# Kernel optimization log

Hardware: AMD Instinct MI355X
Metric: run time of the kernel (lower is better)

The kernel has to match this reference:

```python
import jax, jax.numpy as jnp
import numpy as np

L, d, D, X, B = 64, 2, 32, 2, 2048  # sites, local dim, bond dim, kraus dim, batch
STD = 0.01  # kernel_init = normal(stddev=0.01)


def setup_inputs() -> dict:
    key = jax.random.key(0)
    k1, k2, k3, k4 = jax.random.split(key, 4)
    # local quantum-number indices for (row, col) halves: shape [B, 2L]
    qn = jax.random.randint(k1, (B, 2 * L), 0, d, dtype=jnp.int32)
    # boundary tensors: random + all-ones boundary (as in setup())
    left = STD * jax.random.normal(k2, (d, D, X), jnp.float32) + jnp.ones((d, D, X), jnp.float32)
    right = STD * jax.random.normal(k3, (d, D, X), jnp.float32) + jnp.ones((d, D, X), jnp.float32)
    # middle tensors: random + identity on the (D,D) bond indices for every (site, s, kraus)
    iden = jnp.broadcast_to(jnp.eye(D, dtype=jnp.float32)[None, None, :, :, None], (L - 2, d, D, D, X))
    middle = STD * jax.random.normal(k4, (L - 2, d, D, D, X), jnp.float32) + iden
    return {"qn": qn, "left_tensors": left, "right_tensors": right, "middle_tensors": middle}


def _contract_mpdo(qn, left_tensors, right_tensors, middle_tensors):
    # qn: [2L] ints; split into row / column quantum numbers of the density matrix
    qn_r, qn_c = jnp.split(qn, 2, axis=-1)
    # left/right boundary edges: (D,X) @ (X,D) -> (D,D)
    left_edge = left_tensors[qn_r[0]] @ jnp.conj(left_tensors[qn_c[0]]).T
    right_edge = right_tensors[qn_r[-1]] @ jnp.conj(right_tensors[qn_c[-1]]).T

    @jax.checkpoint
    def step(edge, pair):
        tensor, sr, sc = pair  # tensor: (d,D,D,X)
        # (D,D,X) x (D,D) -> (D,X,D)
        tri = jnp.einsum('ijk,il->jkl', tensor[sr], edge)
        # (D,X,D) x (D,D,X) -> (D,D)
        new_edge = jnp.einsum('jkl,lmk->jm', tri, jnp.conj(tensor[sc]))
        return new_edge, None

    edge, _ = jax.lax.scan(step, left_edge, (middle_tensors, qn_r[1:-1], qn_c[1:-1]), unroll=1)
    return jnp.einsum('ij,ij->', edge, right_edge)


def reference(qn, left_tensors, right_tensors, middle_tensors):
    rho = jax.vmap(lambda q: _contract_mpdo(q, left_tensors, right_tensors, middle_tensors))(qn)
    return jnp.log(rho.astype(jnp.complex64))
```

## Files before the change

### kernel.cpp

```cpp
#include <hip/hip_runtime.h>
#include <hip/hip_bf16.h>
#include <math.h>


typedef __attribute__((ext_vector_type(8)))  short short8;
typedef __attribute__((ext_vector_type(16))) float f32x16;

#define EPITCH 33

static __device__ inline unsigned pk2(float lo, float hi) {
    union { __hip_bfloat162 h; unsigned u; } cv;
    cv.h = __float22bfloat162_rn(make_float2(lo, hi));
    return cv.u;
}
static __device__ inline short8 mk8(unsigned u0, unsigned u1, unsigned u2, unsigned u3) {
    union { short8 v; unsigned u[4]; } r;
    r.u[0] = u0; r.u[1] = u1; r.u[2] = u2; r.u[3] = u3;
    return r.v;
}
static __device__ inline short8 S8(uint4 u) {
    union { uint4 a; short8 v; } c; c.a = u; return c.v;
}
static __device__ inline void pl32swap(unsigned& x, unsigned& y) {
    asm("v_permlane32_swap_b32 %0, %1" : "+v"(x), "+v"(y));
}
static __device__ inline f32x16 MFMA(short8 a, short8 b, f32x16 c) {
    return __builtin_amdgcn_mfma_f32_32x32x16_bf16(a, b, c, 0, 0, 0);
}
static __device__ inline f32x16 zero16() {
    f32x16 z = {0.f,0.f,0.f,0.f,0.f,0.f,0.f,0.f,0.f,0.f,0.f,0.f,0.f,0.f,0.f,0.f};
    return z;
}

__global__ __launch_bounds__(256) void mpdo_prestage(
    const float* __restrict__ middle, unsigned* __restrict__ ws)
{
    const int site = blockIdx.x;
    const int t    = threadIdx.x;
    const int s    = t >> 7;
    const int h    = (t >> 6) & 1;
    const int hi   = (t >> 5) & 1;
    const int col  = t & 31;
    const float2* m2 = (const float2*)middle + (size_t)(site*2 + s) * 1024;
    float2 v[8];
    #pragma unroll
    for (int e = 0; e < 8; ++e) {
        const int kk = 16*h + 8*hi + e;
        float2 d = m2[kk*32 + col];
        if (kk == col) { d.x -= 1.f; d.y -= 1.f; }
        v[e] = d;
    }
    uint4 o0, o1;
    o0.x = pk2(v[0].x, v[1].x); o0.y = pk2(v[2].x, v[3].x);
    o0.z = pk2(v[4].x, v[5].x); o0.w = pk2(v[6].x, v[7].x);
    o1.x = pk2(v[0].y, v[1].y); o1.y = pk2(v[2].y, v[3].y);
    o1.z = pk2(v[4].y, v[5].y); o1.w = pk2(v[6].y, v[7].y);
    uint4* w4 = (uint4*)ws;
    const int lane_off = hi*32 + col;
    w4[((site*2 + s)*4 + 0 + h)*64 + lane_off] = o0;
    w4[((site*2 + s)*4 + 2 + h)*64 + lane_off] = o1;
}

#define SITE_BODY(CA, CB, NA, NB, SITE)                                          \
  {                                                                              \
        \
    float ef[16];                                                                \
    _Pragma("unroll")                                                            \
    for (int h = 0; h < 2; ++h) {                                                \
      const int base = col*EPITCH + 16*h + 8*hi;                                 \
      _Pragma("unroll")                                                          \
      for (int c = 0; c < 8; ++c) ef[h*8 + c] = Ew[base + c];                    \
    }                                                                            \
                                                  \
    short8 EB[2];                                                                \
    _Pragma("unroll")                                                            \
    for (int h = 0; h < 2; ++h) {                                                \
      unsigned ua = pk2(e[8*h+0], e[8*h+1]);                                     \
      unsigned ub = pk2(e[8*h+2], e[8*h+3]);                                     \
      unsigned uc = pk2(e[8*h+4], e[8*h+5]);                                     \
      unsigned ud = pk2(e[8*h+6], e[8*h+7]);                                     \
      pl32swap(ua, uc); pl32swap(ub, ud);                                        \
      EB[h] = mk8(ua, ub, uc, ud);                                               \
    }                                                                            \
                                                              \
    f32x16 acc0 = MFMA(S8(CA[0]), EB[0], zero16());                              \
    acc0 = MFMA(S8(CA[1]), EB[1], acc0);                                         \
    f32x16 acc1 = MFMA(S8(CA[2]), EB[0], zero16());                              \
    acc1 = MFMA(S8(CA[3]), EB[1], acc1);                                         \
                                                                    \
    short8 EA[2];                                                                \
    _Pragma("unroll")                                                            \
    for (int h = 0; h < 2; ++h)                                                  \
      EA[h] = mk8(pk2(ef[8*h+0], ef[8*h+1]), pk2(ef[8*h+2], ef[8*h+3]),          \
                  pk2(ef[8*h+4], ef[8*h+5]), pk2(ef[8*h+6], ef[8*h+7]));         \
                                                                \
    f32x16 V0 = MFMA(EA[0], S8(CB[0]), zero16());                                \
    V0 = MFMA(EA[1], S8(CB[1]), V0);                                             \
    f32x16 V1 = MFMA(EA[0], S8(CB[2]), zero16());                                \
    V1 = MFMA(EA[1], S8(CB[3]), V1);                                             \
                            \
    {                                                                            \
      const int pfi = ((SITE) < 62) ? (SITE) : 61;                               \
      const int ba = (pfi*2 + srn)*4, bb = (pfi*2 + scn)*4;                      \
      _Pragma("unroll")                                                          \
      for (int kh = 0; kh < 4; ++kh) {                                           \
        NA[kh] = w4g[(ba + kh)*64 + lane_off];                                   \
        NB[kh] = w4g[(bb + kh)*64 + lane_off];                                   \
      }                                                                          \
      const int qi = ((SITE) + 2 <= 62) ? (SITE) + 2 : 62;                       \
      srn = q[qi]; scn = q[qi + 64];                                             \
    }                                                                            \
                                             \
    _Pragma("unroll")                                                            \
    for (int h = 0; h < 2; ++h) {                                                \
      unsigned ua = pk2(V0[8*h+0], V0[8*h+1]);                                   \
      unsigned ub = pk2(V0[8*h+2], V0[8*h+3]);                                   \
      unsigned uc = pk2(V0[8*h+4], V0[8*h+5]);                                   \
      unsigned ud = pk2(V0[8*h+6], V0[8*h+7]);                                   \
      pl32swap(ua, uc); pl32swap(ub, ud);                                        \
      acc0 = MFMA(S8(CA[h]), mk8(ua, ub, uc, ud), acc0);                         \
    }                                                                            \
    _Pragma("unroll")                                                            \
    for (int h = 0; h < 2; ++h) {                                                \
      unsigned ua = pk2(V1[8*h+0], V1[8*h+1]);                                   \
      unsigned ub = pk2(V1[8*h+2], V1[8*h+3]);                                   \
      unsigned uc = pk2(V1[8*h+4], V1[8*h+5]);                                   \
      unsigned ud = pk2(V1[8*h+6], V1[8*h+7]);                                   \
      pl32swap(ua, uc); pl32swap(ub, ud);                                        \
      acc1 = MFMA(S8(CA[2+h]), mk8(ua, ub, uc, ud), acc1);                       \
    }                                                                            \
          \
    _Pragma("unroll")                                                            \
    for (int r = 0; r < 16; ++r)                                                 \
      e[r] = fmaf(2.f, e[r], (acc0[r] + acc1[r]) + (V0[r] + V1[r]));             \
    _Pragma("unroll")                                                            \
    for (int r = 0; r < 16; ++r) Ew[rowr[r]*EPITCH + col] = e[r];                \
  }

__global__ __launch_bounds__(256, 2) void mpdo_ws(
    const int*      __restrict__ qn,
    const float*    __restrict__ left,
    const float*    __restrict__ right,
    const unsigned* __restrict__ ws,
    float*          __restrict__ out,
    const int       cplx)
{
    __shared__ float E_all[4][32*EPITCH];

    const int t    = threadIdx.x;
    const int w    = t >> 6;
    const int lane = t & 63;
    const int hi   = lane >> 5;
    const int col  = lane & 31;
    const int elem = blockIdx.x * 4 + w;
    const int* q   = qn + (size_t)elem * 128;
    float* Ew = E_all[w];
    const int lane_off = hi*32 + col;
    const uint4* w4g = (const uint4*)ws;

    int rowr[16];
    #pragma unroll
    for (int r = 0; r < 16; ++r) rowr[r] = (r & 3) + 8*(r >> 2) + 4*hi;

    float e[16];
    {
        const float* Lr = left + (size_t)q[0]  * 64;
        const float* Lc = left + (size_t)q[64] * 64;
        const float c0v = Lc[col*2 + 0], c1v = Lc[col*2 + 1];
        #pragma unroll
        for (int r = 0; r < 16; ++r)
            e[r] = Lr[rowr[r]*2 + 0] * c0v + Lr[rowr[r]*2 + 1] * c1v;
    }
    #pragma unroll
    for (int r = 0; r < 16; ++r) Ew[rowr[r]*EPITCH + col] = e[r];

    uint4 CA[4], CB[4], NA[4], NB[4];
    {
        const int sr = q[1], sc = q[65];
        const int ba = sr*4, bb = sc*4;
        #pragma unroll
        for (int kh = 0; kh < 4; ++kh) {
            CA[kh] = w4g[(ba + kh)*64 + lane_off];
            CB[kh] = w4g[(bb + kh)*64 + lane_off];
        }
    }
    int srn = q[2], scn = q[66];

    #pragma unroll 1
    for (int it = 0; it < 31; ++it) {
        const int siteA = 2*it + 1;
        SITE_BODY(CA, CB, NA, NB, siteA)
        SITE_BODY(NA, NB, CA, CB, siteA + 1)
    }

    {
        const float* Rr = right + (size_t)q[63]  * 64;
        const float* Rc = right + (size_t)q[127] * 64;
        const float rc0 = Rc[col*2 + 0], rc1 = Rc[col*2 + 1];
        float part = 0.f;
        #pragma unroll
        for (int r = 0; r < 16; ++r) {
            const float re = Rr[rowr[r]*2 + 0]*rc0 + Rr[rowr[r]*2 + 1]*rc1;
            part += e[r] * re;
        }
        #pragma unroll
        for (int off = 32; off > 0; off >>= 1)
            part += __shfl_down(part, off, 64);
        if (lane == 0) {
            const float re = logf(fabsf(part));
            if (cplx) {
                out[2*elem + 0] = re;
                out[2*elem + 1] = (part < 0.f) ? 3.14159265358979323846f : 0.f;
            } else {
                out[elem] = re;
            }
        }
    }
}

__global__ __launch_bounds__(256, 2) void mpdo_mfma_fb(
    const int* __restrict__ qn, const float* __restrict__ left,
    const float* __restrict__ right, const float* __restrict__ middle,
    float* __restrict__ out, const int cplx)
{
    __shared__ unsigned mid_b[2048];
    __shared__ float    E_s[4][32*EPITCH];

    const int t = threadIdx.x, w = t >> 6, lane = t & 63;
    const int hi = lane >> 5, col = lane & 31;
    const int elem = blockIdx.x * 4 + w;
    const int* q = qn + (size_t)elem * 128;
    float* Ew = E_s[w];
    const int sp = (t >> 4) & 15, sj = t & 15, jj = sj * 2;
    const float dj = (sp == sj) ? 1.0f : 0.0f;
    const int v0 = (0 + 2*sp) * 16 + sj, v1 = (32 + 2*sp) * 16 + sj;

    int rowr[16];
    #pragma unroll
    for (int r = 0; r < 16; ++r) rowr[r] = (r & 3) + 8*(r >> 2) + 4*hi;

    float e[16];
    {
        const float* Lr = left + (size_t)q[0]  * 64;
        const float* Lc = left + (size_t)q[64] * 64;
        const float c0v = Lc[col*2 + 0], c1v = Lc[col*2 + 1];
        #pragma unroll
        for (int r = 0; r < 16; ++r)
            e[r] = Lr[rowr[r]*2 + 0] * c0v + Lr[rowr[r]*2 + 1] * c1v;
    }
    const float4* gm = (const float4*)middle;
    float4 A0 = gm[v0], A1 = gm[v0 + 16], B0 = gm[v1], B1 = gm[v1 + 16];
    int srn = q[1], scn = q[65];

    for (int site = 1; site <= 62; ++site) {
        {
            uint2* m2 = (uint2*)mid_b;
            m2[((0*16 + sp)*32 + jj) >> 1] = make_uint2(pk2(A0.x - dj, A1.x), pk2(A0.z, A1.z - dj));
            m2[((1*16 + sp)*32 + jj) >> 1] = make_uint2(pk2(A0.y - dj, A1.y), pk2(A0.w, A1.w - dj));
            m2[((2*16 + sp)*32 + jj) >> 1] = make_uint2(pk2(B0.x - dj, B1.x), pk2(B0.z, B1.z - dj));
            m2[((3*16 + sp)*32 + jj) >> 1] = make_uint2(pk2(B0.y - dj, B1.y), pk2(B0.w, B1.w - dj));
        }
        #pragma unroll
        for (int r = 0; r < 16; ++r) Ew[rowr[r]*EPITCH + col] = e[r];
        __syncthreads();
        const int sr = srn, sc = scn;
        if (site < 62) {
            const float4* gn = (const float4*)(middle + (size_t)site * 4096);
            A0 = gn[v0]; A1 = gn[v0 + 16]; B0 = gn[v1]; B1 = gn[v1 + 16];
            srn = q[site + 1]; scn = q[site + 65];
        }
        short8 aT[2][2], bF[2][2];
        #pragma unroll
        for (int k = 0; k < 2; ++k)
            #pragma unroll
            for (int h = 0; h < 2; ++h) {
                const int pa = ((sr*2 + k)*16 + 8*h + 4*hi) * 32 + col;
                aT[k][h] = mk8(mid_b[pa], mid_b[pa+32], mid_b[pa+64], mid_b[pa+96]);
                const int pb = ((sc*2 + k)*16 + 8*h + 4*hi) * 32 + col;
                bF[k][h] = mk8(mid_b[pb], mid_b[pb+32], mid_b[pb+64], mid_b[pb+96]);
            }
        short8 EA[2];
        #pragma unroll
        for (int h = 0; h < 2; ++h) {
            const int base = col*EPITCH + 16*h + 8*hi;
            EA[h] = mk8(pk2(Ew[base+0], Ew[base+1]), pk2(Ew[base+2], Ew[base+3]),
                        pk2(Ew[base+4], Ew[base+5]), pk2(Ew[base+6], Ew[base+7]));
        }
        short8 EB[2];
        #pragma unroll
        for (int h = 0; h < 2; ++h) {
            unsigned ua = pk2(e[8*h+0], e[8*h+1]);
            unsigned ub = pk2(e[8*h+2], e[8*h+3]);
            unsigned uc = pk2(e[8*h+4], e[8*h+5]);
            unsigned ud = pk2(e[8*h+6], e[8*h+7]);
            pl32swap(ua, uc); pl32swap(ub, ud);
            EB[h] = mk8(ua, ub, uc, ud);
        }
        f32x16 V0 = MFMA(EA[0], bF[0][0], zero16()); V0 = MFMA(EA[1], bF[0][1], V0);
        f32x16 V1 = MFMA(EA[0], bF[1][0], zero16()); V1 = MFMA(EA[1], bF[1][1], V1);
        f32x16 acc = MFMA(aT[0][0], EB[0], zero16());
        acc = MFMA(aT[0][1], EB[1], acc);
        acc = MFMA(aT[1][0], EB[0], acc);
        acc = MFMA(aT[1][1], EB[1], acc);
        #pragma unroll
        for (int k = 0; k < 2; ++k) {
            const f32x16& V = k ? V1 : V0;
            #pragma unroll
            for (int h = 0; h < 2; ++h) {
                unsigned ua = pk2(V[8*h+0], V[8*h+1]);
                unsigned ub = pk2(V[8*h+2], V[8*h+3]);
                unsigned uc = pk2(V[8*h+4], V[8*h+5]);
                unsigned ud = pk2(V[8*h+6], V[8*h+7]);
                pl32swap(ua, uc); pl32swap(ub, ud);
                acc = MFMA(aT[k][h], mk8(ua, ub, uc, ud), acc);
            }
        }
        #pragma unroll
        for (int r = 0; r < 16; ++r)
            e[r] = 2.0f*e[r] + acc[r] + V0[r] + V1[r];
        __syncthreads();
    }
    {
        const float* Rr = right + (size_t)q[63]  * 64;
        const float* Rc = right + (size_t)q[127] * 64;
        const float rc0 = Rc[col*2 + 0], rc1 = Rc[col*2 + 1];
        float part = 0.f;
        #pragma unroll
        for (int r = 0; r < 16; ++r)
            part += e[r] * (Rr[rowr[r]*2 + 0]*rc0 + Rr[rowr[r]*2 + 1]*rc1);
        #pragma unroll
        for (int off = 32; off > 0; off >>= 1)
            part += __shfl_down(part, off, 64);
        if (lane == 0) {
            const float re = logf(fabsf(part));
            if (cplx) { out[2*elem] = re; out[2*elem+1] = (part < 0.f) ? 3.14159265f : 0.f; }
            else      { out[elem] = re; }
        }
    }
}

extern "C" void kernel_launch(void* const* d_in, const int* in_sizes, int n_in,
                              void* d_out, int out_size, void* d_ws, size_t ws_size,
                              hipStream_t stream) {
    const int*   qn     = (const int*)  d_in[0];
    const float* left   = (const float*)d_in[1];
    const float* right  = (const float*)d_in[2];
    const float* middle = (const float*)d_in[3];
    float* out = (float*)d_out;

    const int B    = in_sizes[0] / 128;
    const int cplx = (out_size >= 2 * B) ? 1 : 0;
    const size_t need = 62ull * 8192ull;

    if (ws_size >= need) {
        mpdo_prestage<<<62, 256, 0, stream>>>(middle, (unsigned*)d_ws);
        mpdo_ws<<<B / 4, 256, 0, stream>>>(qn, left, right, (const unsigned*)d_ws,
                                           out, cplx);
    } else {
        mpdo_mfma_fb<<<B / 4, 256, 0, stream>>>(qn, left, right, middle, out, cplx);
    }
}
```

Baseline: 129.2 us.

## Carry edge and its transpose in registers instead of round-tripping through LDS

```diff
diff --git a/kernel.cpp b/kernel.cpp
--- a/kernel.cpp
+++ b/kernel.cpp
@@ -5,8 +5,6 @@
 
 typedef __attribute__((ext_vector_type(8)))  short short8;
 typedef __attribute__((ext_vector_type(16))) float f32x16;
-
-#define EPITCH 33
 
 static __device__ inline unsigned pk2(float lo, float hi) {
     union { __hip_bfloat162 h; unsigned u; } cv;
@@ -30,6 +28,28 @@
 static __device__ inline f32x16 zero16() {
     f32x16 z = {0.f,0.f,0.f,0.f,0.f,0.f,0.f,0.f,0.f,0.f,0.f,0.f,0.f,0.f,0.f,0.f};
     return z;
+}
+static __device__ inline void packS(const float* s, short8* out) {
+    #pragma unroll
+    for (int h = 0; h < 2; ++h) {
+        unsigned ua = pk2(s[8*h+0], s[8*h+1]);
+        unsigned ub = pk2(s[8*h+2], s[8*h+3]);
+        unsigned uc = pk2(s[8*h+4], s[8*h+5]);
+        unsigned ud = pk2(s[8*h+6], s[8*h+7]);
+        pl32swap(ua, uc); pl32swap(ub, ud);
+        out[h] = mk8(ua, ub, uc, ud);
+    }
+}
+static __device__ inline void packV(const f32x16& v, short8* out) {
+    #pragma unroll
+    for (int h = 0; h < 2; ++h) {
+        unsigned ua = pk2(v[8*h+0], v[8*h+1]);
+        unsigned ub = pk2(v[8*h+2], v[8*h+3]);
+        unsigned uc = pk2(v[8*h+4], v[8*h+5]);
+        unsigned ud = pk2(v[8*h+6], v[8*h+7]);
+        pl32swap(ua, uc); pl32swap(ub, ud);
+        out[h] = mk8(ua, ub, uc, ud);
+    }
 }
 
 __global__ __launch_bounds__(256) void mpdo_prestage(
@@ -63,42 +83,30 @@
 
 #define SITE_BODY(CA, CB, NA, NB, SITE)                                          \
   {                                                                              \
-        \
-    float ef[16];                                                                \
-    _Pragma("unroll")                                                            \
-    for (int h = 0; h < 2; ++h) {                                                \
-      const int base = col*EPITCH + 16*h + 8*hi;                                 \
-      _Pragma("unroll")                                                          \
-      for (int c = 0; c < 8; ++c) ef[h*8 + c] = Ew[base + c];                    \
-    }                                                                            \
-                                                  \
-    short8 EB[2];                                                                \
-    _Pragma("unroll")                                                            \
-    for (int h = 0; h < 2; ++h) {                                                \
-      unsigned ua = pk2(e[8*h+0], e[8*h+1]);                                     \
-      unsigned ub = pk2(e[8*h+2], e[8*h+3]);                                     \
-      unsigned uc = pk2(e[8*h+4], e[8*h+5]);                                     \
-      unsigned ud = pk2(e[8*h+6], e[8*h+7]);                                     \
-      pl32swap(ua, uc); pl32swap(ub, ud);                                        \
-      EB[h] = mk8(ua, ub, uc, ud);                                               \
-    }                                                                            \
-                                                              \
-    f32x16 acc0 = MFMA(S8(CA[0]), EB[0], zero16());                              \
-    acc0 = MFMA(S8(CA[1]), EB[1], acc0);                                         \
-    f32x16 acc1 = MFMA(S8(CA[2]), EB[0], zero16());                              \
-    acc1 = MFMA(S8(CA[3]), EB[1], acc1);                                         \
-                                                                    \
-    short8 EA[2];                                                                \
-    _Pragma("unroll")                                                            \
-    for (int h = 0; h < 2; ++h)                                                  \
-      EA[h] = mk8(pk2(ef[8*h+0], ef[8*h+1]), pk2(ef[8*h+2], ef[8*h+3]),          \
-                  pk2(ef[8*h+4], ef[8*h+5]), pk2(ef[8*h+6], ef[8*h+7]));         \
-                                                                \
+    short8 EB[2], EA[2];                                                         \
+    packS(e, EB);                                                                \
+    packS(f, EA);                                                                \
+                             \
+    f32x16 accP = MFMA(S8(CA[0]), EB[0], zero16());                              \
+    accP = MFMA(S8(CA[1]), EB[1], accP);                                         \
+    accP = MFMA(S8(CA[2]), EB[0], accP);                                         \
+    accP = MFMA(S8(CA[3]), EB[1], accP);                                         \
+                                                     \
+    f32x16 accQ = MFMA(S8(CB[0]), EA[0], zero16());                              \
+    accQ = MFMA(S8(CB[1]), EA[1], accQ);                                         \
+    accQ = MFMA(S8(CB[2]), EA[0], accQ);                                         \
+    accQ = MFMA(S8(CB[3]), EA[1], accQ);                                         \
+                                      \
     f32x16 V0 = MFMA(EA[0], S8(CB[0]), zero16());                                \
     V0 = MFMA(EA[1], S8(CB[1]), V0);                                             \
     f32x16 V1 = MFMA(EA[0], S8(CB[2]), zero16());                                \
     V1 = MFMA(EA[1], S8(CB[3]), V1);                                             \
-                            \
+                                       \
+    f32x16 Gs = MFMA(EB[0], S8(CA[0]), zero16());                                \
+    Gs = MFMA(EB[1], S8(CA[1]), Gs);                                             \
+    Gs = MFMA(EB[0], S8(CA[2]), Gs);                                             \
+    Gs = MFMA(EB[1], S8(CA[3]), Gs);                                             \
+                                             \
     {                                                                            \
       const int pfi = ((SITE) < 62) ? (SITE) : 61;                               \
       const int ba = (pfi*2 + srn)*4, bb = (pfi*2 + scn)*4;                      \
@@ -110,34 +118,29 @@
       const int qi = ((SITE) + 2 <= 62) ? (SITE) + 2 : 62;                       \
       srn = q[qi]; scn = q[qi + 64];                                             \
     }                                                                            \
-                                             \
+                 \
+    {                                                                            \
+      short8 VB[2];                                                              \
+      packV(V0, VB);                                                             \
+      accP = MFMA(S8(CA[0]), VB[0], accP);                                       \
+      accP = MFMA(S8(CA[1]), VB[1], accP);                                       \
+      accQ = MFMA(VB[0], S8(CA[0]), accQ);                                       \
+      accQ = MFMA(VB[1], S8(CA[1]), accQ);                                       \
+      packV(V1, VB);                                                             \
+      accP = MFMA(S8(CA[2]), VB[0], accP);                                       \
+      accP = MFMA(S8(CA[3]), VB[1], accP);                                       \
+      accQ = MFMA(VB[0], S8(CA[2]), accQ);                                       \
+      accQ = MFMA(VB[1], S8(CA[3]), accQ);                                       \
+    }                                                                            \
+                                                                    \
     _Pragma("unroll")                                                            \
-    for (int h = 0; h < 2; ++h) {                                                \
-      unsigned ua = pk2(V0[8*h+0], V0[8*h+1]);                                   \
-      unsigned ub = pk2(V0[8*h+2], V0[8*h+3]);                                   \
-      unsigned uc = pk2(V0[8*h+4], V0[8*h+5]);                                   \
-      unsigned ud = pk2(V0[8*h+6], V0[8*h+7]);                                   \
-      pl32swap(ua, uc); pl32swap(ub, ud);                                        \
-      acc0 = MFMA(S8(CA[h]), mk8(ua, ub, uc, ud), acc0);                         \
+    for (int r = 0; r < 16; ++r) {                                               \
+      e[r] = fmaf(2.f, e[r], (accP[r] + V0[r]) + V1[r]);                         \
+      f[r] = fmaf(2.f, f[r], accQ[r] + Gs[r]);                                   \
     }                                                                            \
-    _Pragma("unroll")                                                            \
-    for (int h = 0; h < 2; ++h) {                                                \
-      unsigned ua = pk2(V1[8*h+0], V1[8*h+1]);                                   \
-      unsigned ub = pk2(V1[8*h+2], V1[8*h+3]);                                   \
-      unsigned uc = pk2(V1[8*h+4], V1[8*h+5]);                                   \
-      unsigned ud = pk2(V1[8*h+6], V1[8*h+7]);                                   \
-      pl32swap(ua, uc); pl32swap(ub, ud);                                        \
-      acc1 = MFMA(S8(CA[2+h]), mk8(ua, ub, uc, ud), acc1);                       \
-    }                                                                            \
-          \
-    _Pragma("unroll")                                                            \
-    for (int r = 0; r < 16; ++r)                                                 \
-      e[r] = fmaf(2.f, e[r], (acc0[r] + acc1[r]) + (V0[r] + V1[r]));             \
-    _Pragma("unroll")                                                            \
-    for (int r = 0; r < 16; ++r) Ew[rowr[r]*EPITCH + col] = e[r];                \
   }
 
-__global__ __launch_bounds__(256, 2) void mpdo_ws(
+__global__ __launch_bounds__(256, 2) void mpdo_dual(
     const int*      __restrict__ qn,
     const float*    __restrict__ left,
     const float*    __restrict__ right,
@@ -145,8 +148,6 @@
     float*          __restrict__ out,
     const int       cplx)
 {
-    __shared__ float E_all[4][32*EPITCH];
-
     const int t    = threadIdx.x;
     const int w    = t >> 6;
     const int lane = t & 63;
@@ -154,7 +155,6 @@
     const int col  = lane & 31;
     const int elem = blockIdx.x * 4 + w;
     const int* q   = qn + (size_t)elem * 128;
-    float* Ew = E_all[w];
     const int lane_off = hi*32 + col;
     const uint4* w4g = (const uint4*)ws;
 
@@ -162,17 +162,18 @@
     #pragma unroll
     for (int r = 0; r < 16; ++r) rowr[r] = (r & 3) + 8*(r >> 2) + 4*hi;
 
-    float e[16];
+    float e[16], f[16];
     {
         const float* Lr = left + (size_t)q[0]  * 64;
         const float* Lc = left + (size_t)q[64] * 64;
         const float c0v = Lc[col*2 + 0], c1v = Lc[col*2 + 1];
-        #pragma unroll
-        for (int r = 0; r < 16; ++r)
+        const float d0v = Lr[col*2 + 0], d1v = Lr[col*2 + 1];
+        #pragma unroll
+        for (int r = 0; r < 16; ++r) {
             e[r] = Lr[rowr[r]*2 + 0] * c0v + Lr[rowr[r]*2 + 1] * c1v;
-    }
-    #pragma unroll
-    for (int r = 0; r < 16; ++r) Ew[rowr[r]*EPITCH + col] = e[r];
+            f[r] = Lc[rowr[r]*2 + 0] * d0v + Lc[rowr[r]*2 + 1] * d1v;
+        }
+    }
 
     uint4 CA[4], CB[4], NA[4], NB[4];
     {
@@ -218,6 +219,7 @@
     }
 }
 
+#define EPITCH 33
 __global__ __launch_bounds__(256, 2) void mpdo_mfma_fb(
     const int* __restrict__ qn, const float* __restrict__ left,
     const float* __restrict__ right, const float* __restrict__ middle,
@@ -287,15 +289,7 @@
                         pk2(Ew[base+4], Ew[base+5]), pk2(Ew[base+6], Ew[base+7]));
         }
         short8 EB[2];
-        #pragma unroll
-        for (int h = 0; h < 2; ++h) {
-            unsigned ua = pk2(e[8*h+0], e[8*h+1]);
-            unsigned ub = pk2(e[8*h+2], e[8*h+3]);
-            unsigned uc = pk2(e[8*h+4], e[8*h+5]);
-            unsigned ud = pk2(e[8*h+6], e[8*h+7]);
-            pl32swap(ua, uc); pl32swap(ub, ud);
-            EB[h] = mk8(ua, ub, uc, ud);
-        }
+        packS(e, EB);
         f32x16 V0 = MFMA(EA[0], bF[0][0], zero16()); V0 = MFMA(EA[1], bF[0][1], V0);
         f32x16 V1 = MFMA(EA[0], bF[1][0], zero16()); V1 = MFMA(EA[1], bF[1][1], V1);
         f32x16 acc = MFMA(aT[0][0], EB[0], zero16());
@@ -304,16 +298,10 @@
         acc = MFMA(aT[1][1], EB[1], acc);
         #pragma unroll
         for (int k = 0; k < 2; ++k) {
-            const f32x16& V = k ? V1 : V0;
-            #pragma unroll
-            for (int h = 0; h < 2; ++h) {
-                unsigned ua = pk2(V[8*h+0], V[8*h+1]);
-                unsigned ub = pk2(V[8*h+2], V[8*h+3]);
-                unsigned uc = pk2(V[8*h+4], V[8*h+5]);
-                unsigned ud = pk2(V[8*h+6], V[8*h+7]);
-                pl32swap(ua, uc); pl32swap(ub, ud);
-                acc = MFMA(aT[k][h], mk8(ua, ub, uc, ud), acc);
-            }
+            short8 VB[2];
+            packV(k ? V1 : V0, VB);
+            acc = MFMA(aT[k][0], VB[0], acc);
+            acc = MFMA(aT[k][1], VB[1], acc);
         }
         #pragma unroll
         for (int r = 0; r < 16; ++r)
@@ -354,8 +342,8 @@
 
     if (ws_size >= need) {
         mpdo_prestage<<<62, 256, 0, stream>>>(middle, (unsigned*)d_ws);
-        mpdo_ws<<<B / 4, 256, 0, stream>>>(qn, left, right, (const unsigned*)d_ws,
-                                           out, cplx);
+        mpdo_dual<<<B / 4, 256, 0, stream>>>(qn, left, right, (const unsigned*)d_ws,
+                                             out, cplx);
     } else {
         mpdo_mfma_fb<<<B / 4, 256, 0, stream>>>(qn, left, right, middle, out, cplx);
     }
```

Measured after the change: 150.9 us. 1.17x slower.
